# Performance work log

Hardware: AMD Instinct MI355X
Metric: run time of the kernel (lower is better)

Reference implementation:

```python
import jax, jax.numpy as jnp
import jax.scipy.linalg as jsl
import numpy as np

EPS = 1e-7            # torchvision iou-loss eps
GIOU_THRESHOLD = 0.2
MIN_VARIANCE = 1e-6


def cxcywh_to_xyxy(b):
    cx, cy, w, h = b[..., 0], b[..., 1], b[..., 2], b[..., 3]
    return jnp.stack([cx - 0.5 * w, cy - 0.5 * h, cx + 0.5 * w, cy + 0.5 * h], axis=-1)


def kalman_filtered_boxes(prev_boxes, prev_logits, image_sizes, swp, sws, log_q_diag):
    # scale: [B,1,4] = [w,h,w,h] for denormalization
    scale = jnp.stack([image_sizes[:, 1], image_sizes[:, 0], image_sizes[:, 1], image_sizes[:, 0]], axis=-1)[:, None, :]
    box_abs = prev_boxes * scale                               # [B,Q,4] absolute cxcywh
    conf = jax.nn.softmax(prev_logits, axis=-1).max(axis=-1)   # [B,Q]
    # predict step: P_pred = F P0 F^T + Q  (track-independent 8x8)
    idx = jnp.arange(4)
    F = jnp.eye(8, dtype=box_abs.dtype).at[idx, idx + 4].set(1.0)
    P0 = jnp.diag(jnp.array([100.0] * 4 + [1000.0] * 4, dtype=box_abs.dtype))
    Qm = jnp.diag(jnp.exp(log_q_diag))
    P_pred = F @ P0 @ F.T + Qm                                 # [8,8]
    # detection covariance R per track (DetectionCovarianceGate)
    hc = jnp.maximum(box_abs[..., 3], 1.0)
    std = jnp.stack([swp * hc, swp * hc, sws * hc, sws * hc], axis=-1)
    std = std / jnp.maximum(conf, 1e-6)[..., None]
    std = jnp.maximum(std, 0.1)
    eye4 = jnp.eye(4, dtype=box_abs.dtype)
    R = eye4 * (std ** 2)[..., None, :] + MIN_VARIANCE * eye4  # [B,Q,4,4]
    # innovation covariance, gain via batched Cholesky + triangular solves
    S = P_pred[:4, :4] + R + MIN_VARIANCE * eye4               # [B,Q,4,4]
    L = jnp.linalg.cholesky(S)
    covHT_T = jnp.broadcast_to(P_pred[:, :4].T, S.shape[:-2] + (4, 8))
    y = jsl.solve_triangular(L, covHT_T, lower=True)
    Kt = jsl.solve_triangular(jnp.swapaxes(L, -1, -2), y, lower=False)
    K = jnp.swapaxes(Kt, -1, -2)                               # [B,Q,8,4]
    # state init from the same box + zero velocity -> F @ mean0 = [box; 0]
    mean_pred = jnp.concatenate([box_abs, jnp.zeros_like(box_abs)], axis=-1)  # [B,Q,8]
    innovation = box_abs - mean_pred[..., :4]  # identically zero; kept faithful to original
    mean_new = mean_pred + jnp.einsum('bqij,bqj->bqi', K, innovation)
    return mean_new[..., :4] / scale


def pairwise_giou_loss(p, t):
    # p: [B,Q,4], t: [B,T,4] in xyxy -> [B,Q,T] GIoU loss
    a = p[:, :, None, :]
    b = t[:, None, :, :]
    area_a = (a[..., 2] - a[..., 0]) * (a[..., 3] - a[..., 1])
    area_b = (b[..., 2] - b[..., 0]) * (b[..., 3] - b[..., 1])
    lt = jnp.maximum(a[..., :2], b[..., :2])
    rb = jnp.minimum(a[..., 2:], b[..., 2:])
    wh = jnp.maximum(rb - lt, 0.0)
    inter = wh[..., 0] * wh[..., 1]
    union = area_a + area_b - inter
    iou = inter / (union + EPS)
    ltc = jnp.minimum(a[..., :2], b[..., :2])
    rbc = jnp.maximum(a[..., 2:], b[..., 2:])
    whc = jnp.maximum(rbc - ltc, 0.0)
    area_c = whc[..., 0] * whc[..., 1]
    giou = iou - (area_c - union) / (area_c + EPS)
    return 1.0 - giou


def ciou_loss_mean(p, t):
    # elementwise complete-IoU loss (torchvision semantics), mean-reduced
    x1, y1, x2, y2 = p[..., 0], p[..., 1], p[..., 2], p[..., 3]
    xg1, yg1, xg2, yg2 = t[..., 0], t[..., 1], t[..., 2], t[..., 3]
    iw = jnp.maximum(jnp.minimum(x2, xg2) - jnp.maximum(x1, xg1), 0.0)
    ih = jnp.maximum(jnp.minimum(y2, yg2) - jnp.maximum(y1, yg1), 0.0)
    inter = iw * ih
    union = (x2 - x1) * (y2 - y1) + (xg2 - xg1) * (yg2 - yg1) - inter
    iou = inter / (union + EPS)
    cw = jnp.maximum(x2, xg2) - jnp.minimum(x1, xg1)
    ch = jnp.maximum(y2, yg2) - jnp.minimum(y1, yg1)
    c2 = cw ** 2 + ch ** 2 + EPS
    d2 = ((x1 + x2 - xg1 - xg2) ** 2 + (y1 + y2 - yg1 - yg2) ** 2) / 4.0
    v = (4.0 / (jnp.pi ** 2)) * (jnp.arctan((xg2 - xg1) / (yg2 - yg1)) - jnp.arctan((x2 - x1) / (y2 - y1))) ** 2
    alpha = jax.lax.stop_gradient(v / (1.0 - iou + v + EPS))
    return jnp.mean(1.0 - iou + d2 / c2 + alpha * v)


def _hungarian(cost):
    # O(n^3) shortest-augmenting-path Hungarian (min-cost square assignment).
    # Returns col assignment for rows 0..n-1 (rows are implicitly arange(n)).
    n = cost.shape[0]
    u = np.zeros(n + 1)
    v = np.zeros(n + 1)
    p = np.zeros(n + 1, dtype=np.int64)
    way = np.zeros(n + 1, dtype=np.int64)
    for i in range(1, n + 1):
        p[0] = i
        j0 = 0
        minv = np.full(n + 1, np.inf)
        used = np.zeros(n + 1, dtype=bool)
        while True:
            used[j0] = True
            i0 = p[j0]
            js = np.nonzero(~used)[0]
            js = js[js > 0]
            cur = cost[i0 - 1, js - 1] - u[i0] - v[js]
            upd = cur < minv[js]
            minv[js] = np.minimum(minv[js], cur)
            way[js[upd]] = j0
            j1 = js[int(np.argmin(minv[js]))]
            delta = minv[j1]
            uj = np.nonzero(used)[0]
            u[p[uj]] += delta
            v[uj] -= delta
            minv[js] -= delta
            j0 = j1
            if p[j0] == 0:
                break
        while j0 != 0:
            j1 = way[j0]
            p[j0] = p[j1]
            j0 = j1
    col_of_row = np.empty(n, dtype=np.int64)
    for j in range(1, n + 1):
        col_of_row[p[j] - 1] = j - 1
    return col_of_row


def setup_inputs() -> dict:
    key = jax.random.key(0)
    k = jax.random.split(key, 4)
    B, Q, C = 8, 512, 92
    prev_boxes = jax.random.uniform(k[0], (B, Q, 4), jnp.float32)
    prev_logits = jax.random.normal(k[1], (B, Q, C), jnp.float32)
    curr_boxes = jax.random.uniform(k[2], (B, Q, 4), jnp.float32)
    image_sizes = jax.random.uniform(k[3], (B, 2), jnp.float32) * 800.0 + 480.0
    return {
        'prev_boxes': prev_boxes,
        'prev_logits': prev_logits,
        'curr_boxes': curr_boxes,
        'image_sizes': image_sizes,
        'std_weight_position': jnp.asarray(0.05, jnp.float32),
        'std_weight_size': jnp.asarray(0.05, jnp.float32),
        'log_q_diag': jnp.log(jnp.array([0.01] * 4 + [1e-4] * 4, jnp.float32)),
    }


def reference(prev_boxes, prev_logits, curr_boxes, image_sizes, std_weight_position, std_weight_size, log_q_diag):
    filtered = kalman_filtered_boxes(prev_boxes, prev_logits, image_sizes,
                                     std_weight_position, std_weight_size, log_q_diag)
    # Hungarian matching on thresholded pairwise GIoU-loss cost (no-grad in original)
    gl = pairwise_giou_loss(cxcywh_to_xyxy(curr_boxes), cxcywh_to_xyxy(filtered))  # [B,Q,Q]
    cost = np.asarray(jax.lax.stop_gradient(gl) < GIOU_THRESHOLD, dtype=np.float64)
    cols = jnp.asarray(np.stack([_hungarian(cost[b]) for b in range(cost.shape[0])]))
    # original: matched_preds = pred[col_indices]; matched_targets = target[row_indices] (rows=arange)
    matched_preds = jnp.take_along_axis(curr_boxes, cols[..., None], axis=1)
    matched_targets = filtered
    return ciou_loss_mean(cxcywh_to_xyxy(matched_preds), cxcywh_to_xyxy(matched_targets))
```

## Files before the change

kernel.cpp:

```cpp
#include <hip/hip_runtime.h>
#include <stdint.h>
#include <math.h>

#define NB 8
#define NQ 512

typedef unsigned long long u64;

static __device__ __forceinline__ u64 getw8(const u64 (&a)[8], int w) {
    u64 r = 0ull;
#pragma unroll
    for (int k = 0; k < 8; k++) if (k == w) r = a[k];
    return r;
}
static __device__ __forceinline__ void setbit8(u64 (&a)[8], int c) {
    int w = c >> 6; u64 m = 1ull << (c & 63);
#pragma unroll
    for (int k = 0; k < 8; k++) if (k == w) a[k] |= m;
}
static __device__ __forceinline__ bool getbit8(const u64 (&a)[8], int c) {
    return (getw8(a, c >> 6) >> (c & 63)) & 1ull;
}

__global__ void cost_kernel(const float* __restrict__ prev_boxes,
                            const float* __restrict__ curr_boxes,
                            const float* __restrict__ image_sizes,
                            u64* __restrict__ cost,
                            float* __restrict__ out) {
#pragma clang fp contract(off)
    int t = blockIdx.x * blockDim.x + threadIdx.x;
    if (t == 0) out[0] = 0.f;
    int b = t >> 18;
    int rem = t & (NQ * NQ - 1);
    int i = rem >> 9;
    int j = rem & (NQ - 1);
    float4 cb = ((const float4*)curr_boxes)[(b << 9) + i];
    float ax = cb.x - 0.5f * cb.z, ay = cb.y - 0.5f * cb.w;
    float az = cb.x + 0.5f * cb.z, aw = cb.y + 0.5f * cb.w;
    float H = image_sizes[2 * b + 0];
    float W = image_sizes[2 * b + 1];
    float4 pb = ((const float4*)prev_boxes)[(b << 9) + j];
    float fcx = (pb.x * W) / W, fcy = (pb.y * H) / H;
    float fw  = (pb.z * W) / W, fh  = (pb.w * H) / H;
    float bx = fcx - 0.5f * fw, by = fcy - 0.5f * fh;
    float bz = fcx + 0.5f * fw, bw = fcy + 0.5f * fh;
    float area_a = (az - ax) * (aw - ay);
    float area_b = (bz - bx) * (bw - by);
    float ltx = fmaxf(ax, bx), lty = fmaxf(ay, by);
    float rbx = fminf(az, bz), rby = fminf(aw, bw);
    float w = fmaxf(rbx - ltx, 0.f), h = fmaxf(rby - lty, 0.f);
    float inter = w * h;
    float uni = area_a + area_b - inter;
    float iou = inter / (uni + 1e-7f);
    float lcx = fminf(ax, bx), lcy = fminf(ay, by);
    float rcx = fmaxf(az, bz), rcy = fmaxf(aw, bw);
    float wc = fmaxf(rcx - lcx, 0.f), hc = fmaxf(rcy - lcy, 0.f);
    float areac = wc * hc;
    float giou = iou - (areac - uni) / (areac + 1e-7f);
    float gl = 1.f - giou;
    u64 m = __ballot(gl < 0.2f);
    if ((threadIdx.x & 63) == 0)
        cost[((size_t)((b << 9) + i)) * 8 + (j >> 6)] = m;
}

__global__ __launch_bounds__(256, 1) void hungarian_kernel(
        const u64* __restrict__ cost,
        const float* __restrict__ prev_boxes,
        const float* __restrict__ curr_boxes,
        const float* __restrict__ image_sizes,
        float* __restrict__ out) {
    int b = blockIdx.x;
    int tid = threadIdx.x;
    int lane = tid & 63;
    int wv = tid >> 6;
    __shared__ __align__(16) u64 costL[NQ * 8];
    __shared__ int p[NQ + 1];
    __shared__ int wayL[NQ + 1];
    __shared__ int u[NQ + 1];
    __shared__ int vv[NQ + 1];
    __shared__ int minvA[NQ + 1];
    __shared__ unsigned char used[NQ + 1];
    __shared__ u64 nzS[8], c0S[8], dgS[8], apS[8], zcS[8];
    __shared__ int actionS;

    {
        const ulonglong2* src = (const ulonglong2*)(cost + (size_t)b * NQ * 8);
        ulonglong2* dst = (ulonglong2*)costL;
        for (int k = tid; k < NQ * 4; k += 256) dst[k] = src[k];
    }
    for (int k = tid; k <= NQ; k += 256) { p[k] = k; wayL[k] = 0; u[k] = 0; vv[k] = 0; }
    __syncthreads();

#pragma unroll
    for (int gi = 0; gi < 2; gi++) {
        int g = 2 * wv + gi;
        const u64* Zr = costL + (((g << 6) + lane) << 3);
        u64 o = 0ull;
#pragma unroll
        for (int k = 0; k < 8; k++) o |= Zr[k];
        u64 nzb = __ballot(o != 0ull);
        u64 c0b = __ballot((Zr[0] & 1ull) != 0ull);
        u64 dgb = __ballot(((Zr[g] >> lane) & 1ull) != 0ull);
        if (lane == 0) { nzS[g] = nzb; c0S[g] = c0b; dgS[g] = dgb; apS[g] = 0ull; }
    }
    __syncthreads();

    u64 nzB[8], c0B[8], dgB[8], apB[8];
    bool ownerNZ0 = false;
    int owner0 = 1;
    u64 Zc[8];
    int wIdx = 0;
    u64 bits = 0ull, pendMask = ~0ull;
    bool started = false;
    if (tid == 0) {
#pragma unroll
        for (int k = 0; k < 8; k++) { nzB[k] = nzS[k]; c0B[k] = c0S[k]; dgB[k] = dgS[k]; apB[k] = 0ull; Zc[k] = 0ull; }
    }

    auto intW = [&](int w) -> u64 {
        u64 x = getw8(c0B, w) | getw8(dgB, w);
        if (ownerNZ0) x |= getw8(apB, w);
        return getw8(nzB, w) & x;
    };
    auto runGeneral = [&](int igen) {
        for (int j = igen; j <= NQ; j++) p[j] = 0;
        for (int i2 = igen; i2 <= NQ; i2++) {
            p[0] = i2;
            for (int j = 0; j <= NQ; j++) { minvA[j] = 0x7fffffff; used[j] = 0; }
            int j0 = 0;
            while (true) {
                used[j0] = 1;
                int i0 = p[j0];
                int ui0 = u[i0];
                const u64* rr = costL + ((size_t)(i0 - 1) << 3);
                int delta = 0x7fffffff, j1 = 0;
                for (int j = 1; j <= NQ; j++) {
                    if (!used[j]) {
                        int cbit = (int)((rr[(j - 1) >> 6] >> ((j - 1) & 63)) & 1ull);
                        int cur = cbit - ui0 - vv[j];
                        if (cur < minvA[j]) { minvA[j] = cur; wayL[j] = (i2 << 10) | j0; }
                        if (minvA[j] < delta) { delta = minvA[j]; j1 = j; }
                    }
                }
                for (int j = 0; j <= NQ; j++) {
                    if (used[j]) { u[p[j]] += delta; vv[j] -= delta; }
                    else minvA[j] -= delta;
                }
                j0 = j1;
                if (p[j0] == 0) break;
            }
            while (j0) {
                int wv2 = wayL[j0];
                int jn = ((wv2 >> 10) == i2) ? (wv2 & 1023) : 0;
                p[j0] = p[jn];
                j0 = jn;
            }
        }
    };

    for (;;) {
        if (tid == 0) {
            int action = 0;
            if (!started) {
                started = true;
                if (nzB[0] & 1ull) {
                    u64 Z1[8];
#pragma unroll
                    for (int k = 0; k < 8; k++) Z1[k] = costL[k];
                    if (!(Z1[0] & 1ull)) {
                        owner0 = 1; ownerNZ0 = true;
#pragma unroll
                        for (int k = 0; k < 8; k++) Zc[k] = Z1[k];
                        action = 1; pendMask = ~1ull; wIdx = 0;
                    } else {
                        runGeneral(1); action = 3;
                    }
                } else {
                    bits = intW(0) & ~1ull;
                }
            }
            while (action == 0) {
                if (bits == 0ull) {
                    wIdx++;
                    if (wIdx >= 8) { action = 3; break; }
                    bits = intW(wIdx);
                    continue;
                }
                int l = __builtin_ctzll(bits);
                bits &= bits - 1;
                u64 rem = (l == 63) ? 0ull : (~0ull << (l + 1));
                int i = (wIdx << 6) + l + 1;
                bool c0 = (getw8(c0B, wIdx) >> l) & 1ull;
                bool apb = ownerNZ0 && ((getw8(apB, wIdx) >> l) & 1ull);
                if (!c0 && !apb) {
                    p[i] = owner0;
                    p[1] = i;
                    owner0 = i; ownerNZ0 = true;
#pragma unroll
                    for (int k = 0; k < 8; k++) Zc[k] = costL[((i - 1) << 3) + k];
                    action = 1; pendMask = rem;
                } else {
                    int prevO = owner0; bool prevF = ownerNZ0;
                    bool bail = false, hole = false;
                    u64 Z[8];
#pragma unroll
                    for (int k = 0; k < 8; k++) Z[k] = costL[((i - 1) << 3) + k];
                    u64 ones[8], vis[8], nzA[8], nzBf[8];
#pragma unroll
                    for (int k = 0; k < 8; k++) { ones[k] = Z[k]; vis[k] = 0ull; nzA[k] = 0ull; nzBf[k] = 0ull; }
                    int fA_c = 0, fA_p = 0, fB_c = 0, fB_p = 0;
                    int foldn = 0, assignTo = -1;
                    while (true) {
                        int c2 = -1;
#pragma unroll
                        for (int k = 7; k >= 0; k--) {
                            u64 s = ~ones[k] & ~vis[k];
                            if (s != 0ull) c2 = (k << 6) + __builtin_ctzll(s);
                        }
                        if (c2 < 0) { bail = true; break; }
                        if (c2 >= i - 1) {
                            if (c2 == i - 1) assignTo = c2;
                            else hole = true;
                            break;
                        }
                        int pc = p[c2 + 1];
                        u64 Zo[8];
#pragma unroll
                        for (int k = 0; k < 8; k++) Zo[k] = costL[((pc - 1) << 3) + k];
                        setbit8(vis, c2);
                        u64 nzv[8], ap2 = 0ull;
#pragma unroll
                        for (int k = 0; k < 8; k++) { nzv[k] = ones[k] & ~Zo[k]; ones[k] &= Zo[k]; ap2 |= ones[k]; }
                        if (foldn == 0) {
                            fA_c = c2; fA_p = pc;
#pragma unroll
                            for (int k = 0; k < 8; k++) nzA[k] = nzv[k];
                        } else if (foldn == 1) {
                            fB_c = c2; fB_p = pc;
#pragma unroll
                            for (int k = 0; k < 8; k++) nzBf[k] = nzv[k];
                        } else {
#pragma unroll
                            for (int k = 0; k < 8; k++) {
                                u64 tt = nzv[k];
                                while (tt) { int b2 = __builtin_ctzll(tt); tt &= tt - 1; wayL[(k << 6) + b2 + 1] = (i << 10) | (c2 + 1); }
                            }
                        }
                        foldn++;
                        if (ap2 == 0ull) { assignTo = i - 1; break; }
                    }
                    if (bail || hole) {
                        runGeneral(i);
                        action = 3;
                    } else {
                        int cc = assignTo;
                        while (true) {
                            bool inA = getbit8(nzA, cc), inB = getbit8(nzBf, cc);
                            if (inB)      { p[cc + 1] = fB_p; cc = fB_c; }
                            else if (inA) { p[cc + 1] = fA_p; cc = fA_c; }
                            else if (foldn > 2) {
                                int wv2 = wayL[cc + 1];
                                if ((wv2 >> 10) == i) { int jn = wv2 & 1023; p[cc + 1] = p[jn]; cc = jn - 1; }
                                else                  { p[cc + 1] = i; break; }
                            } else { p[cc + 1] = i; break; }
                        }
                        owner0 = p[1];
                        ownerNZ0 = (getw8(nzB, (owner0 - 1) >> 6) >> ((owner0 - 1) & 63)) & 1ull;
                        if (ownerNZ0 && !(prevF && prevO == owner0)) {
#pragma unroll
                            for (int k = 0; k < 8; k++) Zc[k] = costL[((owner0 - 1) << 3) + k];
                            action = 1; pendMask = rem;
                        } else {
                            bits = intW(wIdx) & rem;
                        }
                    }
                }
            }
            if (action == 1) {
#pragma unroll
                for (int k = 0; k < 8; k++) zcS[k] = Zc[k];
            }
            actionS = action;
        }
        __syncthreads();
        int action = actionS;
        if (action == 1) {
            u64 zc[8];
#pragma unroll
            for (int k = 0; k < 8; k++) zc[k] = zcS[k];
#pragma unroll
            for (int gi = 0; gi < 2; gi++) {
                int g = 2 * wv + gi;
                const u64* Zr = costL + (((g << 6) + lane) << 3);
                u64 a = 0ull;
#pragma unroll
                for (int k = 0; k < 8; k++) a |= Zr[k] & zc[k];
                u64 bal = __ballot(a != 0ull);
                if (lane == 0) apS[g] = bal;
            }
            __syncthreads();
            if (tid == 0) {
#pragma unroll
                for (int k = 0; k < 8; k++) apB[k] = apS[k];
                ownerNZ0 = true;
                bits = intW(wIdx) & pendMask;
            }
            continue;
        }
        break;
    }
    __syncthreads();

    {
#pragma clang fp contract(off)
        float H = image_sizes[2 * b + 0];
        float W = image_sizes[2 * b + 1];
        float sum = 0.f;
#pragma unroll
        for (int k = 0; k < 2; k++) {
            int j = 1 + tid + (k << 8);
            int r = p[j] - 1;
            int c = j - 1;
            float4 cb = ((const float4*)curr_boxes)[(b << 9) + c];
            float x1 = cb.x - 0.5f * cb.z, y1 = cb.y - 0.5f * cb.w;
            float x2 = cb.x + 0.5f * cb.z, y2 = cb.y + 0.5f * cb.w;
            float4 pb = ((const float4*)prev_boxes)[(b << 9) + r];
            float fcx = (pb.x * W) / W, fcy = (pb.y * H) / H;
            float fw2 = (pb.z * W) / W, fh2 = (pb.w * H) / H;
            float xg1 = fcx - 0.5f * fw2, yg1 = fcy - 0.5f * fh2;
            float xg2 = fcx + 0.5f * fw2, yg2 = fcy + 0.5f * fh2;
            float iw = fmaxf(fminf(x2, xg2) - fmaxf(x1, xg1), 0.f);
            float ih = fmaxf(fminf(y2, yg2) - fmaxf(y1, yg1), 0.f);
            float inter = iw * ih;
            float uni = (x2 - x1) * (y2 - y1) + (xg2 - xg1) * (yg2 - yg1) - inter;
            float iou = inter / (uni + 1e-7f);
            float cw2 = fmaxf(x2, xg2) - fminf(x1, xg1);
            float ch2 = fmaxf(y2, yg2) - fminf(y1, yg1);
            float c2 = cw2 * cw2 + ch2 * ch2 + 1e-7f;
            float dx = ((x1 + x2) - xg1) - xg2;
            float dy = ((y1 + y2) - yg1) - yg2;
            float d2 = (dx * dx + dy * dy) / 4.f;
            const float CC = (float)(4.0 / (M_PI * M_PI));
            float at = atanf((xg2 - xg1) / (yg2 - yg1)) - atanf((x2 - x1) / (y2 - y1));
            float v = CC * (at * at);
            float alpha = v / (((1.f - iou) + v) + 1e-7f);
            sum += ((1.f - iou) + d2 / c2) + alpha * v;
        }
#pragma unroll
        for (int off = 32; off >= 1; off >>= 1) sum += __shfl_xor(sum, off, 64);
        if (lane == 0) atomicAdd(out, sum * (1.f / 4096.f));
    }
}

extern "C" void kernel_launch(void* const* d_in, const int* in_sizes, int n_in,
                              void* d_out, int out_size, void* d_ws, size_t ws_size,
                              hipStream_t stream) {
    const float* prev_boxes  = (const float*)d_in[0];
    const float* curr_boxes  = (const float*)d_in[2];
    const float* image_sizes = (const float*)d_in[3];

    u64* cost = (u64*)d_ws;
    float* out = (float*)d_out;

    cost_kernel<<<(NB * NQ * NQ) / 256, 256, 0, stream>>>(
        prev_boxes, curr_boxes, image_sizes, cost, out);
    hungarian_kernel<<<NB, 256, 0, stream>>>(
        cost, prev_boxes, curr_boxes, image_sizes, out);
}
```

Measured before the change: 80.66 us.

## Store cost bitmatrix word-major and skip already-scanned groups in adjacency update

Changes the packed cost bitmask layout from row-major (row, word) to word-major (word, row) in both the cost kernel and the shared-memory copy, so lanes reading consecutive rows for the same word hit consecutive addresses and avoid LDS bank conflicts in the ballot scans. The parallel adjacency update now skips row groups below the current scan word, because their bits are no longer consulted. The serial thread paths that read full rows now use strided accesses, which may cost a little in the single-thread section.

```diff
diff --git a/kernel.cpp b/kernel.cpp
--- a/kernel.cpp
+++ b/kernel.cpp
@@ -6,6 +6,8 @@
 #define NQ 512
 
 typedef unsigned long long u64;
+
+#define CW(k, r) costL[((k) << 9) + (r)]
 
 static __device__ __forceinline__ u64 getw8(const u64 (&a)[8], int w) {
     u64 r = 0ull;
@@ -60,7 +62,7 @@
     float gl = 1.f - giou;
     u64 m = __ballot(gl < 0.2f);
     if ((threadIdx.x & 63) == 0)
-        cost[((size_t)((b << 9) + i)) * 8 + (j >> 6)] = m;
+        cost[(size_t)b * (NQ * 8) + ((size_t)(j >> 6) << 9) + i] = m;
 }
 
 __global__ __launch_bounds__(256, 1) void hungarian_kernel(
@@ -82,6 +84,7 @@
     __shared__ unsigned char used[NQ + 1];
     __shared__ u64 nzS[8], c0S[8], dgS[8], apS[8], zcS[8];
     __shared__ int actionS;
+    __shared__ int wIdxS;
 
     {
         const ulonglong2* src = (const ulonglong2*)(cost + (size_t)b * NQ * 8);
@@ -94,13 +97,18 @@
 #pragma unroll
     for (int gi = 0; gi < 2; gi++) {
         int g = 2 * wv + gi;
-        const u64* Zr = costL + (((g << 6) + lane) << 3);
-        u64 o = 0ull;
-#pragma unroll
-        for (int k = 0; k < 8; k++) o |= Zr[k];
+        int r = (g << 6) + lane;
+        u64 o = 0ull, w0 = 0ull, wg = 0ull;
+#pragma unroll
+        for (int k = 0; k < 8; k++) {
+            u64 x = CW(k, r);
+            o |= x;
+            if (k == 0) w0 = x;
+            if (k == g) wg = x;
+        }
         u64 nzb = __ballot(o != 0ull);
-        u64 c0b = __ballot((Zr[0] & 1ull) != 0ull);
-        u64 dgb = __ballot(((Zr[g] >> lane) & 1ull) != 0ull);
+        u64 c0b = __ballot((w0 & 1ull) != 0ull);
+        u64 dgb = __ballot(((wg >> lane) & 1ull) != 0ull);
         if (lane == 0) { nzS[g] = nzb; c0S[g] = c0b; dgS[g] = dgb; apS[g] = 0ull; }
     }
     __syncthreads();
@@ -132,11 +140,10 @@
                 used[j0] = 1;
                 int i0 = p[j0];
                 int ui0 = u[i0];
-                const u64* rr = costL + ((size_t)(i0 - 1) << 3);
                 int delta = 0x7fffffff, j1 = 0;
                 for (int j = 1; j <= NQ; j++) {
                     if (!used[j]) {
-                        int cbit = (int)((rr[(j - 1) >> 6] >> ((j - 1) & 63)) & 1ull);
+                        int cbit = (int)((CW((j - 1) >> 6, i0 - 1) >> ((j - 1) & 63)) & 1ull);
                         int cur = cbit - ui0 - vv[j];
                         if (cur < minvA[j]) { minvA[j] = cur; wayL[j] = (i2 << 10) | j0; }
                         if (minvA[j] < delta) { delta = minvA[j]; j1 = j; }
@@ -166,7 +173,7 @@
                 if (nzB[0] & 1ull) {
                     u64 Z1[8];
 #pragma unroll
-                    for (int k = 0; k < 8; k++) Z1[k] = costL[k];
+                    for (int k = 0; k < 8; k++) Z1[k] = CW(k, 0);
                     if (!(Z1[0] & 1ull)) {
                         owner0 = 1; ownerNZ0 = true;
 #pragma unroll
@@ -197,14 +204,14 @@
                     p[1] = i;
                     owner0 = i; ownerNZ0 = true;
 #pragma unroll
-                    for (int k = 0; k < 8; k++) Zc[k] = costL[((i - 1) << 3) + k];
+                    for (int k = 0; k < 8; k++) Zc[k] = CW(k, i - 1);
                     action = 1; pendMask = rem;
                 } else {
                     int prevO = owner0; bool prevF = ownerNZ0;
                     bool bail = false, hole = false;
                     u64 Z[8];
 #pragma unroll
-                    for (int k = 0; k < 8; k++) Z[k] = costL[((i - 1) << 3) + k];
+                    for (int k = 0; k < 8; k++) Z[k] = CW(k, i - 1);
                     u64 ones[8], vis[8], nzA[8], nzBf[8];
 #pragma unroll
                     for (int k = 0; k < 8; k++) { ones[k] = Z[k]; vis[k] = 0ull; nzA[k] = 0ull; nzBf[k] = 0ull; }
@@ -226,7 +233,7 @@
                         int pc = p[c2 + 1];
                         u64 Zo[8];
 #pragma unroll
-                        for (int k = 0; k < 8; k++) Zo[k] = costL[((pc - 1) << 3) + k];
+                        for (int k = 0; k < 8; k++) Zo[k] = CW(k, pc - 1);
                         setbit8(vis, c2);
                         u64 nzv[8], ap2 = 0ull;
 #pragma unroll
@@ -268,7 +275,7 @@
                         ownerNZ0 = (getw8(nzB, (owner0 - 1) >> 6) >> ((owner0 - 1) & 63)) & 1ull;
                         if (ownerNZ0 && !(prevF && prevO == owner0)) {
 #pragma unroll
-                            for (int k = 0; k < 8; k++) Zc[k] = costL[((owner0 - 1) << 3) + k];
+                            for (int k = 0; k < 8; k++) Zc[k] = CW(k, owner0 - 1);
                             action = 1; pendMask = rem;
                         } else {
                             bits = intW(wIdx) & rem;
@@ -279,6 +286,7 @@
             if (action == 1) {
 #pragma unroll
                 for (int k = 0; k < 8; k++) zcS[k] = Zc[k];
+                wIdxS = wIdx;
             }
             actionS = action;
         }
@@ -288,15 +296,18 @@
             u64 zc[8];
 #pragma unroll
             for (int k = 0; k < 8; k++) zc[k] = zcS[k];
+            int w0 = wIdxS;
 #pragma unroll
             for (int gi = 0; gi < 2; gi++) {
                 int g = 2 * wv + gi;
-                const u64* Zr = costL + (((g << 6) + lane) << 3);
-                u64 a = 0ull;
-#pragma unroll
-                for (int k = 0; k < 8; k++) a |= Zr[k] & zc[k];
-                u64 bal = __ballot(a != 0ull);
-                if (lane == 0) apS[g] = bal;
+                if (g >= w0) {
+                    int r = (g << 6) + lane;
+                    u64 a = 0ull;
+#pragma unroll
+                    for (int k = 0; k < 8; k++) a |= CW(k, r) & zc[k];
+                    u64 bal = __ballot(a != 0ull);
+                    if (lane == 0) apS[g] = bal;
+                }
             }
             __syncthreads();
             if (tid == 0) {
```

Result: faster. 78.96 us (-2.1%).
